# Kernel optimization log

Measured on AMD Instinct MI355X. Metric: run time of the kernel, lower is better.

Reference implementation:

```python
import jax, jax.numpy as jnp
import numpy as np

NUM_HEADS = 8
SIGMA = 1.0
LAMBDA_INIT = 0.1
GAMMA_INIT = 0.001


def _pos_encoding(H, W, d_model):
    # 2D sinusoidal encoding: first half encodes x (width), second half y (height)
    d = d_model // 2
    div = jnp.exp(jnp.arange(0, d, 2, dtype=jnp.float32) * (-np.log(10000.0) / d))
    xs = jnp.arange(W, dtype=jnp.float32)[:, None] * div  # (W, d//2)
    ys = jnp.arange(H, dtype=jnp.float32)[:, None] * div  # (H, d//2)
    pe_x = jnp.stack([jnp.sin(xs), jnp.cos(xs)], axis=-1).reshape(W, d)
    pe_y = jnp.stack([jnp.sin(ys), jnp.cos(ys)], axis=-1).reshape(H, d)
    pe = jnp.concatenate([
        jnp.broadcast_to(pe_x[None, :, :], (H, W, d)),
        jnp.broadcast_to(pe_y[:, None, :], (H, W, d)),
    ], axis=-1)
    return pe  # (H, W, d_model)


def _distance_map(H, W, sigma):
    # exp(-euclidean_dist / sigma) between all flattened pixel positions
    yy, xx = jnp.meshgrid(jnp.arange(H, dtype=jnp.float32), jnp.arange(W, dtype=jnp.float32), indexing='ij')
    coords = jnp.stack([yy.reshape(-1), xx.reshape(-1)], axis=-1)  # (HW, 2)
    d2 = jnp.sum((coords[:, None, :] - coords[None, :, :]) ** 2, axis=-1)
    return jnp.exp(-jnp.sqrt(d2) / sigma)  # (HW, HW)


def _conv1x1(x, w, b):
    # 1x1 conv == channel matmul; x: (B,C,H,W), w: (O,C), b: (O,)
    return jnp.einsum('bchw,oc->bohw', x, w) + b[None, :, None, None]


def setup_inputs() -> dict:
    key = jax.random.key(0)
    ks = jax.random.split(key, 9)
    B, C, H, W = 2, 256, 48, 48
    d_model = 256
    inp = {
        'x': jax.random.normal(ks[0], (B, C, H, W), dtype=jnp.float32),
        'Wq': jax.random.normal(ks[1], (d_model, C), dtype=jnp.float32) * 0.01,
        'bq': jnp.zeros((d_model,), dtype=jnp.float32),
        'Wk': jax.random.normal(ks[2], (d_model, C), dtype=jnp.float32) * 0.01,
        'bk': jnp.zeros((d_model,), dtype=jnp.float32),
        'Wv': jax.random.normal(ks[3], (d_model, C), dtype=jnp.float32) * 0.01,
        'bv': jnp.zeros((d_model,), dtype=jnp.float32),
        'Wo': jax.random.normal(ks[4], (C, d_model), dtype=jnp.float32) * 0.01,
        'bo': jnp.zeros((C,), dtype=jnp.float32),
        'lambda_dist': jnp.float32(LAMBDA_INIT),
        'gamma': jnp.float32(GAMMA_INIT),
    }
    return inp


def reference(x, Wq, bq, Wk, bk, Wv, bv, Wo, bo, lambda_dist, gamma):
    B, C, H, W = x.shape
    d_model = Wq.shape[0]
    d_k = d_model // NUM_HEADS
    pe = _pos_encoding(H, W, d_model).transpose(2, 0, 1)[None]  # (1, d_model, H, W)
    dm = _distance_map(H, W, SIGMA)                              # (HW, HW)

    q = _conv1x1(x, Wq, bq) + pe
    k = _conv1x1(x, Wk, bk) + pe
    v = _conv1x1(x, Wv, bv)

    def heads(t):
        return t.reshape(B, NUM_HEADS, d_k, H * W).transpose(0, 1, 3, 2)  # (B,h,HW,d_k)

    Q, K, V = heads(q), heads(k), heads(v)
    scores = jnp.einsum('bhnd,bhmd->bhnm', Q, K) / jnp.sqrt(jnp.float32(d_k))
    scores = scores + (lambda_dist * dm)[None, None]  # 'exp' distance prior bias
    attn = jax.nn.softmax(scores, axis=-1)
    out = jnp.einsum('bhnm,bhmd->bhnd', attn, V)
    out = out.transpose(0, 1, 3, 2).reshape(B, d_model, H, W)
    fused = gamma * out  # simple weighted fusion, single (self) branch
    return x + _conv1x1(fused, Wo, bo)
```

## Files before the change

kernel.cpp:

```cpp
#include <hip/hip_runtime.h>

#define HW 2304
#define SW 48
#define DMODEL 256
#define NHEADS 8
#define DK 32
#define BATCH 2

typedef unsigned short u16;
typedef __attribute__((ext_vector_type(8))) short short8;
typedef __attribute__((ext_vector_type(4))) float f32x4;

__device__ __forceinline__ float bf2f(u16 v) {
  union { unsigned int u; float f; } c; c.u = ((unsigned int)v) << 16; return c.f;
}
__device__ __forceinline__ float lo2f(unsigned int u) {
  union { unsigned int u; float f; } c; c.u = u << 16; return c.f;
}
__device__ __forceinline__ float hi2f(unsigned int u) {
  union { unsigned int u; float f; } c; c.u = u & 0xffff0000u; return c.f;
}
__device__ __forceinline__ u16 f2bf(float f) {
  union { unsigned int u; float f; } c; c.f = f;
  unsigned int u = c.u;
  unsigned int r = (u + 0x7FFFu + ((u >> 16) & 1u)) >> 16;
  return (u16)r;
}
__device__ __forceinline__ int div48(int n) { return (n * 87382) >> 22; }
__device__ __forceinline__ int swz(int row, int k) {
  return ((row >> 4) << 12) + ((k >> 3) << 7) + ((row & 15) << 3) + (k & 7);
}

__global__ __launch_bounds__(256) void eb_kernel(const float* __restrict__ lam_p,
                                                 u16* __restrict__ et) {
  int id = blockIdx.x * 256 + threadIdx.x;
  int flat = id * 8;
  int tile = flat >> 8;
  int within = flat & 255;
  int tm = tile / 144, tq = tile - tm * 144;
  int m = tm * 16 + (within >> 4);
  int q = tq * 16 + (within & 15);
  int ym = div48(m), xm = m - ym * SW;
  int yq = div48(q), xq = q - yq * SW;
  float lam = lam_p[0];
  float dy = (float)(yq - ym);
  float dy2 = dy * dy;
  u16 o[8];
#pragma unroll
  for (int j = 0; j < 8; ++j) {
    float dx = (float)(xq + j - xm);
    o[j] = f2bf(lam * __expf(-sqrtf(dy2 + dx * dx)));
  }
  *(uint4*)(et + flat) = *(const uint4*)o;
}

__global__ __launch_bounds__(256) void prep_kernel(
    const float* __restrict__ x,
    const float* __restrict__ Wq, const float* __restrict__ Wk,
    const float* __restrict__ Wv, const float* __restrict__ Wo,
    u16* __restrict__ xt, u16* __restrict__ Wb) {
  int bid = blockIdx.x;
  int t = threadIdx.x;
  if (bid < 288) {
    int b = bid / 144, r = bid % 144;
    int c0 = (r / 36) * 64, n0 = (r % 36) * 64;
    __shared__ u16 sh[64][72];
#pragma unroll
    for (int p = 0; p < 4; ++p) {
      int row = (t >> 4) + p * 16;
      int col4 = (t & 15) * 4;
      float4 v = *(const float4*)(x + (size_t)(b * DMODEL + c0 + row) * HW +
                                  n0 + col4);
      sh[col4 + 0][row] = f2bf(v.x);
      sh[col4 + 1][row] = f2bf(v.y);
      sh[col4 + 2][row] = f2bf(v.z);
      sh[col4 + 3][row] = f2bf(v.w);
    }
    __syncthreads();
    u16* xtb = xt + (size_t)b * HW * DMODEL;
#pragma unroll
    for (int q = 0; q < 2; ++q) {
      int nrow = t >> 2;
      int c8 = (t & 3) * 8 + q * 32;
      *(uint4*)(xtb + swz(n0 + nrow, c0 + c8)) = *(const uint4*)&sh[nrow][c8];
    }
  } else {
    int idx = (bid - 288) * 1024 + t * 4;
    int which = idx >> 16, off = idx & 65535;
    int m = off >> 8, k = off & 255;
    const float* src = (which == 0) ? Wq : (which == 1) ? Wk
                       : (which == 2) ? Wv : Wo;
    float4 v = *(const float4*)(src + off);
    ushort4 ov;
    ov.x = f2bf(v.x); ov.y = f2bf(v.y); ov.z = f2bf(v.z); ov.w = f2bf(v.w);
    *(ushort4*)(Wb + which * 65536 + swz(m, k)) = ov;
  }
}

__global__ __launch_bounds__(256) void qkv_kernel(
    const u16* __restrict__ Wb, const u16* __restrict__ xt,
    const float* __restrict__ bq, const float* __restrict__ bk,
    const float* __restrict__ bv,
    u16* __restrict__ qt, u16* __restrict__ ktb, u16* __restrict__ vb) {
  int t = threadIdx.x;
  int w = t >> 6, lane = t & 63, lo = lane & 15, quad = lane >> 4;
  int n0 = blockIdx.x * 64;
  int mb = blockIdx.y, b = blockIdx.z;
  int which = mb >> 2;
  int mrel0 = (mb & 3) * 64;
  const u16* A = Wb + which * 65536 + ((mrel0 + w * 16) >> 4) * 4096 + lo * 8;
  const float* bias = (which == 0) ? bq : (which == 1) ? bk : bv;
  const u16* Bx = xt + (size_t)b * HW * DMODEL + lo * 8;

  f32x4 acc[4] = {{0.f, 0.f, 0.f, 0.f}, {0.f, 0.f, 0.f, 0.f},
                  {0.f, 0.f, 0.f, 0.f}, {0.f, 0.f, 0.f, 0.f}};
#pragma unroll
  for (int k0 = 0; k0 < DMODEL; k0 += 32) {
    int kblk = ((k0 >> 3) + quad) << 7;
    short8 af = *(const short8*)(A + kblk);
#pragma unroll
    for (int nt = 0; nt < 4; ++nt) {
      short8 bf_ = *(const short8*)(Bx + ((n0 + nt * 16) >> 4) * 4096 + kblk);
      acc[nt] = __builtin_amdgcn_mfma_f32_16x16x32_bf16(af, bf_, acc[nt], 0, 0, 0);
    }
  }

  int mbase = mrel0 + w * 16 + quad * 4;
  if (which == 2) {
#pragma unroll
    for (int reg = 0; reg < 4; ++reg) {
      int mrel = mbase + reg;
      float bi = bias[mrel];
      u16* dst = vb + (size_t)(b * DMODEL + mrel) * HW + n0 + lo;
#pragma unroll
      for (int nt = 0; nt < 4; ++nt) dst[nt * 16] = f2bf(acc[nt][reg] + bi);
    }
  } else {
    float sc = (which == 0) ? 0.17677669529663687f : 1.0f;
    int h = mbase >> 5, d0 = mbase & 31;
    u16* base = ((which == 0) ? qt : ktb) + (size_t)(b * NHEADS + h) * HW * DK;
    float bi[4], dv[4];
    bool usecos[4], usey[4];
#pragma unroll
    for (int reg = 0; reg < 4; ++reg) {
      int mrel = mbase + reg;
      bi[reg] = bias[mrel];
      int oo = mrel & 127;
      dv[reg] = expf(-0.07195578415606394f * (float)(oo & ~1));
      usecos[reg] = (oo & 1);
      usey[reg] = (mrel >= 128);
    }
#pragma unroll
    for (int nt = 0; nt < 4; ++nt) {
      int n = n0 + nt * 16 + lo;
      int yy = div48(n), xx = n - yy * SW;
      ushort4 ov;
      float vals[4];
#pragma unroll
      for (int reg = 0; reg < 4; ++reg) {
        float tv = (usey[reg] ? (float)yy : (float)xx) * dv[reg];
        float pe = usecos[reg] ? cosf(tv) : sinf(tv);
        vals[reg] = (acc[nt][reg] + bi[reg] + pe) * sc;
      }
      ov.x = f2bf(vals[0]); ov.y = f2bf(vals[1]);
      ov.z = f2bf(vals[2]); ov.w = f2bf(vals[3]);
      *(ushort4*)(base + (size_t)n * DK + d0) = ov;
    }
  }
}

__global__ __launch_bounds__(256) void attn_kernel(
    const u16* __restrict__ qt, const u16* __restrict__ ktb,
    const u16* __restrict__ vb, const u16* __restrict__ et,
    u16* __restrict__ aot) {
  int t = threadIdx.x;
  int w = t >> 6;
  int lane = t & 63;
  int lo = lane & 15, quad = lane >> 4;
  int n0 = blockIdx.x * 64;
  int h = blockIdx.y, b = blockIdx.z;

  __shared__ u16 Ks[64 * 40];
  __shared__ u16 Vs[32 * 72];
  __shared__ u16 Ps[4 * 16 * 72];

  const u16* qtg = qt + (size_t)(b * NHEADS + h) * HW * DK;
  const u16* ktg = ktb + (size_t)(b * NHEADS + h) * HW * DK;
  const u16* vbg = vb + (size_t)(b * DMODEL + h * DK) * HW;

  short8 qf = *(const short8*)(qtg + (size_t)(n0 + w * 16 + lo) * DK + quad * 8);

  int tq = (n0 >> 4) + w;
  const u16* etw = et + (size_t)tq * 256 + lo * 16 + quad * 4;

  f32x4 o0 = {0.f, 0.f, 0.f, 0.f}, o1 = {0.f, 0.f, 0.f, 0.f};
  float lsum[4] = {0.f, 0.f, 0.f, 0.f};
  u16* psw = Ps + w * 16 * 72;

  for (int kt = 0; kt < 36; ++kt) {
    int m0 = kt * 64;
    __syncthreads();
    {
      int row = t >> 2, c8 = (t & 3) * 8;
      *(uint4*)&Ks[row * 40 + c8] =
          *(const uint4*)(ktg + (size_t)(m0 + row) * DK + c8);
      int dd = t >> 3, mo = (t & 7) * 8;
      *(uint4*)&Vs[dd * 72 + mo] =
          *(const uint4*)(vbg + (size_t)dd * HW + m0 + mo);
    }
    __syncthreads();

    uint2 ebv[4];
#pragma unroll
    for (int t4 = 0; t4 < 4; ++t4)
      ebv[t4] = *(const uint2*)(etw + (size_t)((m0 >> 4) + t4) * 36864);

    f32x4 s[4];
#pragma unroll
    for (int t4 = 0; t4 < 4; ++t4) {
      short8 kf = *(const short8*)&Ks[(t4 * 16 + lo) * 40 + quad * 8];
      f32x4 z = {0.f, 0.f, 0.f, 0.f};
      s[t4] = __builtin_amdgcn_mfma_f32_16x16x32_bf16(qf, kf, z, 0, 0, 0);
    }
#pragma unroll
    for (int t4 = 0; t4 < 4; ++t4) {
      float p0 = __expf(s[t4][0] + lo2f(ebv[t4].x));
      float p1 = __expf(s[t4][1] + hi2f(ebv[t4].x));
      float p2 = __expf(s[t4][2] + lo2f(ebv[t4].y));
      float p3 = __expf(s[t4][3] + hi2f(ebv[t4].y));
      lsum[0] += p0; lsum[1] += p1; lsum[2] += p2; lsum[3] += p3;
      psw[(quad * 4 + 0) * 72 + t4 * 16 + lo] = f2bf(p0);
      psw[(quad * 4 + 1) * 72 + t4 * 16 + lo] = f2bf(p1);
      psw[(quad * 4 + 2) * 72 + t4 * 16 + lo] = f2bf(p2);
      psw[(quad * 4 + 3) * 72 + t4 * 16 + lo] = f2bf(p3);
    }
#pragma unroll
    for (int ks = 0; ks < 2; ++ks) {
      short8 af = *(const short8*)&psw[lo * 72 + ks * 32 + quad * 8];
      short8 v0 = *(const short8*)&Vs[lo * 72 + ks * 32 + quad * 8];
      o0 = __builtin_amdgcn_mfma_f32_16x16x32_bf16(af, v0, o0, 0, 0, 0);
      short8 v1 = *(const short8*)&Vs[(16 + lo) * 72 + ks * 32 + quad * 8];
      o1 = __builtin_amdgcn_mfma_f32_16x16x32_bf16(af, v1, o1, 0, 0, 0);
    }
  }

#pragma unroll
  for (int d = 1; d < 16; d <<= 1) {
#pragma unroll
    for (int reg = 0; reg < 4; ++reg) lsum[reg] += __shfl_xor(lsum[reg], d);
  }

  u16* aog = aot + (size_t)b * HW * DMODEL;
#pragma unroll
  for (int reg = 0; reg < 4; ++reg) {
    int n = n0 + w * 16 + quad * 4 + reg;
    float inv = 1.0f / lsum[reg];
    aog[swz(n, h * DK + lo)] = f2bf(o0[reg] * inv);
    aog[swz(n, h * DK + 16 + lo)] = f2bf(o1[reg] * inv);
  }
}

__global__ __launch_bounds__(256) void out_kernel(
    const float* __restrict__ x, const u16* __restrict__ Wob,
    const float* __restrict__ bo, const float* __restrict__ gp,
    const u16* __restrict__ aot, float* __restrict__ out) {
  int t = threadIdx.x;
  int w = t >> 6, lane = t & 63, lo = lane & 15, quad = lane >> 4;
  int n0 = blockIdx.x * 64;
  int c0 = blockIdx.y * 64;
  int b = blockIdx.z;
  float gamma = gp[0];
  const u16* A = Wob + ((c0 + w * 16) >> 4) * 4096 + lo * 8;
  const u16* Ba = aot + (size_t)b * HW * DMODEL + lo * 8;

  f32x4 acc[4] = {{0.f, 0.f, 0.f, 0.f}, {0.f, 0.f, 0.f, 0.f},
                  {0.f, 0.f, 0.f, 0.f}, {0.f, 0.f, 0.f, 0.f}};
#pragma unroll
  for (int k0 = 0; k0 < DMODEL; k0 += 32) {
    int kblk = ((k0 >> 3) + quad) << 7;
    short8 af = *(const short8*)(A + kblk);
#pragma unroll
    for (int nt = 0; nt < 4; ++nt) {
      short8 bf_ = *(const short8*)(Ba + ((n0 + nt * 16) >> 4) * 4096 + kblk);
      acc[nt] = __builtin_amdgcn_mfma_f32_16x16x32_bf16(af, bf_, acc[nt], 0, 0, 0);
    }
  }

#pragma unroll
  for (int reg = 0; reg < 4; ++reg) {
    int c = c0 + w * 16 + quad * 4 + reg;
    float bi = bo[c];
    const float* xs = x + (size_t)(b * DMODEL + c) * HW + n0 + lo;
    float* os = out + (size_t)(b * DMODEL + c) * HW + n0 + lo;
#pragma unroll
    for (int nt = 0; nt < 4; ++nt)
      os[nt * 16] = xs[nt * 16] + gamma * acc[nt][reg] + bi;
  }
}

extern "C" void kernel_launch(void* const* d_in, const int* in_sizes, int n_in,
                              void* d_out, int out_size, void* d_ws,
                              size_t ws_size, hipStream_t stream) {
  const float* x   = (const float*)d_in[0];
  const float* Wq  = (const float*)d_in[1];
  const float* bq  = (const float*)d_in[2];
  const float* Wk  = (const float*)d_in[3];
  const float* bk  = (const float*)d_in[4];
  const float* Wv  = (const float*)d_in[5];
  const float* bv  = (const float*)d_in[6];
  const float* Wo  = (const float*)d_in[7];
  const float* bo  = (const float*)d_in[8];
  const float* lam = (const float*)d_in[9];
  const float* gam = (const float*)d_in[10];

  char* wsb = (char*)d_ws;
  u16* Wb  = (u16*)(wsb + 36864);
  u16* xt  = (u16*)(wsb + 561152);
  u16* aot = xt;
  u16* qt  = (u16*)(wsb + 2920448);
  u16* ktb = (u16*)(wsb + 5279744);
  u16* vb  = (u16*)(wsb + 7639040);
  u16* et  = (u16*)(wsb + 9998336);
  float* out = (float*)d_out;

  eb_kernel<<<dim3(2592), 256, 0, stream>>>(lam, et);
  prep_kernel<<<dim3(544), 256, 0, stream>>>(x, Wq, Wk, Wv, Wo, xt, Wb);
  qkv_kernel<<<dim3(36, 12, BATCH), 256, 0, stream>>>(Wb, xt, bq, bk, bv,
                                                      qt, ktb, vb);
  attn_kernel<<<dim3(36, NHEADS, BATCH), 256, 0, stream>>>(qt, ktb, vb, et,
                                                           aot);
  out_kernel<<<dim3(36, 4, BATCH), 256, 0, stream>>>(x, Wb + 3 * 65536, bo, gam,
                                                     aot, out);
}
```

Before: 151.3 us.

## Load K/V fragments straight into registers with double-buffered prefetch

The attention kernel no longer stages K and V tiles through shared memory with two block-wide barriers per tile. Each wave now loads its MFMA K and V fragments directly from global memory into registers. It alternates between two register buffers so the next tile's loads are in flight while the current tile is computed. The aim is to remove the barrier stalls and LDS round trips and to hide load latency. In exchange, each of the four waves re-reads the same K/V data, which relies on the caches, and register pressure rises. The final prefetch also reads one tile past the end of the sequence.

```diff
diff --git a/kernel.cpp b/kernel.cpp
--- a/kernel.cpp
+++ b/kernel.cpp
@@ -169,6 +169,22 @@
   }
 }
 
+__device__ __forceinline__ void ld_tile(const u16* __restrict__ ktg,
+                                        const u16* __restrict__ vbg, int m0,
+                                        int lo, int quad,
+                                        short8 kf[4], short8 vf[4]) {
+#pragma unroll
+  for (int t4 = 0; t4 < 4; ++t4)
+    kf[t4] = *(const short8*)(ktg + (size_t)(m0 + t4 * 16 + lo) * DK + quad * 8);
+#pragma unroll
+  for (int ks = 0; ks < 2; ++ks) {
+    vf[ks * 2 + 0] =
+        *(const short8*)(vbg + (size_t)lo * HW + m0 + ks * 32 + quad * 8);
+    vf[ks * 2 + 1] =
+        *(const short8*)(vbg + (size_t)(16 + lo) * HW + m0 + ks * 32 + quad * 8);
+  }
+}
+
 __global__ __launch_bounds__(256) void attn_kernel(
     const u16* __restrict__ qt, const u16* __restrict__ ktb,
     const u16* __restrict__ vb, const u16* __restrict__ et,
@@ -180,8 +196,6 @@
   int n0 = blockIdx.x * 64;
   int h = blockIdx.y, b = blockIdx.z;
 
-  __shared__ u16 Ks[64 * 40];
-  __shared__ u16 Vs[32 * 72];
   __shared__ u16 Ps[4 * 16 * 72];
 
   const u16* qtg = qt + (size_t)(b * NHEADS + h) * HW * DK;
@@ -197,52 +211,47 @@
   float lsum[4] = {0.f, 0.f, 0.f, 0.f};
   u16* psw = Ps + w * 16 * 72;
 
-  for (int kt = 0; kt < 36; ++kt) {
-    int m0 = kt * 64;
-    __syncthreads();
-    {
-      int row = t >> 2, c8 = (t & 3) * 8;
-      *(uint4*)&Ks[row * 40 + c8] =
-          *(const uint4*)(ktg + (size_t)(m0 + row) * DK + c8);
-      int dd = t >> 3, mo = (t & 7) * 8;
-      *(uint4*)&Vs[dd * 72 + mo] =
-          *(const uint4*)(vbg + (size_t)dd * HW + m0 + mo);
-    }
-    __syncthreads();
-
-    uint2 ebv[4];
-#pragma unroll
-    for (int t4 = 0; t4 < 4; ++t4)
-      ebv[t4] = *(const uint2*)(etw + (size_t)((m0 >> 4) + t4) * 36864);
-
-    f32x4 s[4];
-#pragma unroll
-    for (int t4 = 0; t4 < 4; ++t4) {
-      short8 kf = *(const short8*)&Ks[(t4 * 16 + lo) * 40 + quad * 8];
-      f32x4 z = {0.f, 0.f, 0.f, 0.f};
-      s[t4] = __builtin_amdgcn_mfma_f32_16x16x32_bf16(qf, kf, z, 0, 0, 0);
-    }
-#pragma unroll
-    for (int t4 = 0; t4 < 4; ++t4) {
-      float p0 = __expf(s[t4][0] + lo2f(ebv[t4].x));
-      float p1 = __expf(s[t4][1] + hi2f(ebv[t4].x));
-      float p2 = __expf(s[t4][2] + lo2f(ebv[t4].y));
-      float p3 = __expf(s[t4][3] + hi2f(ebv[t4].y));
-      lsum[0] += p0; lsum[1] += p1; lsum[2] += p2; lsum[3] += p3;
-      psw[(quad * 4 + 0) * 72 + t4 * 16 + lo] = f2bf(p0);
-      psw[(quad * 4 + 1) * 72 + t4 * 16 + lo] = f2bf(p1);
-      psw[(quad * 4 + 2) * 72 + t4 * 16 + lo] = f2bf(p2);
-      psw[(quad * 4 + 3) * 72 + t4 * 16 + lo] = f2bf(p3);
-    }
-#pragma unroll
-    for (int ks = 0; ks < 2; ++ks) {
-      short8 af = *(const short8*)&psw[lo * 72 + ks * 32 + quad * 8];
-      short8 v0 = *(const short8*)&Vs[lo * 72 + ks * 32 + quad * 8];
-      o0 = __builtin_amdgcn_mfma_f32_16x16x32_bf16(af, v0, o0, 0, 0, 0);
-      short8 v1 = *(const short8*)&Vs[(16 + lo) * 72 + ks * 32 + quad * 8];
-      o1 = __builtin_amdgcn_mfma_f32_16x16x32_bf16(af, v1, o1, 0, 0, 0);
-    }
-  }
+  short8 ka[4], va[4], kb[4], vbf[4];
+  ld_tile(ktg, vbg, 0, lo, quad, ka, va);
+
+#define ATTN_BODY(M0, KF, VF)                                                  \
+  {                                                                            \
+    const int m0_ = (M0);                                                      \
+    uint2 ebv[4];                                                              \
+    _Pragma("unroll") for (int t4 = 0; t4 < 4; ++t4) ebv[t4] =                 \
+        *(const uint2*)(etw + (size_t)((m0_ >> 4) + t4) * 36864);              \
+    f32x4 s[4];                                                                \
+    _Pragma("unroll") for (int t4 = 0; t4 < 4; ++t4) {                         \
+      f32x4 z = {0.f, 0.f, 0.f, 0.f};                                          \
+      s[t4] = __builtin_amdgcn_mfma_f32_16x16x32_bf16(qf, KF[t4], z, 0, 0, 0); \
+    }                                                                          \
+    _Pragma("unroll") for (int t4 = 0; t4 < 4; ++t4) {                         \
+      float p0 = __expf(s[t4][0] + lo2f(ebv[t4].x));                           \
+      float p1 = __expf(s[t4][1] + hi2f(ebv[t4].x));                           \
+      float p2 = __expf(s[t4][2] + lo2f(ebv[t4].y));                           \
+      float p3 = __expf(s[t4][3] + hi2f(ebv[t4].y));                           \
+      lsum[0] += p0; lsum[1] += p1; lsum[2] += p2; lsum[3] += p3;              \
+      psw[(quad * 4 + 0) * 72 + t4 * 16 + lo] = f2bf(p0);                      \
+      psw[(quad * 4 + 1) * 72 + t4 * 16 + lo] = f2bf(p1);                      \
+      psw[(quad * 4 + 2) * 72 + t4 * 16 + lo] = f2bf(p2);                      \
+      psw[(quad * 4 + 3) * 72 + t4 * 16 + lo] = f2bf(p3);                      \
+    }                                                                          \
+    _Pragma("unroll") for (int ks = 0; ks < 2; ++ks) {                         \
+      short8 af = *(const short8*)&psw[lo * 72 + ks * 32 + quad * 8];          \
+      o0 = __builtin_amdgcn_mfma_f32_16x16x32_bf16(af, VF[ks * 2 + 0], o0, 0,  \
+                                                   0, 0);                      \
+      o1 = __builtin_amdgcn_mfma_f32_16x16x32_bf16(af, VF[ks * 2 + 1], o1, 0,  \
+                                                   0, 0);                      \
+    }                                                                          \
+  }
+
+  for (int kt = 0; kt < 36; kt += 2) {
+    ld_tile(ktg, vbg, (kt + 1) * 64, lo, quad, kb, vbf);
+    ATTN_BODY(kt * 64, ka, va);
+    ld_tile(ktg, vbg, (kt + 2) * 64, lo, quad, ka, va);
+    ATTN_BODY((kt + 1) * 64, kb, vbf);
+  }
+#undef ATTN_BODY
 
 #pragma unroll
   for (int d = 1; d < 16; d <<= 1) {
```

Measured after the change: 189.0 us. +25.0%, slower.

## Split attention key range across two blocks and merge partials in reduce kernel

Applied to the files above, without the earlier changes.

The attention kernel now splits the 36 key tiles into two halves handled by separate blocks, doubling the grid to 1152 blocks. Each half writes unnormalised bf16 partial outputs and row sums to scratch space in the output buffer. A new reduce kernel adds the two partials and normalises them. The distance-bias kernel is also folded into the prep kernel, saving one launch. This targets low occupancy, since 576 blocks underfill the GPU, and pays for it with an extra launch, extra global traffic, and bf16 rounding of the partial results. The split has no max-rescaling, which matches the code before, so the softmax runs without max subtraction.

```diff
diff --git a/kernel.cpp b/kernel.cpp
--- a/kernel.cpp
+++ b/kernel.cpp
@@ -31,34 +31,12 @@
   return ((row >> 4) << 12) + ((k >> 3) << 7) + ((row & 15) << 3) + (k & 7);
 }
 
-__global__ __launch_bounds__(256) void eb_kernel(const float* __restrict__ lam_p,
-                                                 u16* __restrict__ et) {
-  int id = blockIdx.x * 256 + threadIdx.x;
-  int flat = id * 8;
-  int tile = flat >> 8;
-  int within = flat & 255;
-  int tm = tile / 144, tq = tile - tm * 144;
-  int m = tm * 16 + (within >> 4);
-  int q = tq * 16 + (within & 15);
-  int ym = div48(m), xm = m - ym * SW;
-  int yq = div48(q), xq = q - yq * SW;
-  float lam = lam_p[0];
-  float dy = (float)(yq - ym);
-  float dy2 = dy * dy;
-  u16 o[8];
-#pragma unroll
-  for (int j = 0; j < 8; ++j) {
-    float dx = (float)(xq + j - xm);
-    o[j] = f2bf(lam * __expf(-sqrtf(dy2 + dx * dx)));
-  }
-  *(uint4*)(et + flat) = *(const uint4*)o;
-}
-
 __global__ __launch_bounds__(256) void prep_kernel(
     const float* __restrict__ x,
     const float* __restrict__ Wq, const float* __restrict__ Wk,
     const float* __restrict__ Wv, const float* __restrict__ Wo,
-    u16* __restrict__ xt, u16* __restrict__ Wb) {
+    const float* __restrict__ lam_p,
+    u16* __restrict__ xt, u16* __restrict__ Wb, u16* __restrict__ et) {
   int bid = blockIdx.x;
   int t = threadIdx.x;
   if (bid < 288) {
@@ -84,7 +62,7 @@
       int c8 = (t & 3) * 8 + q * 32;
       *(uint4*)(xtb + swz(n0 + nrow, c0 + c8)) = *(const uint4*)&sh[nrow][c8];
     }
-  } else {
+  } else if (bid < 544) {
     int idx = (bid - 288) * 1024 + t * 4;
     int which = idx >> 16, off = idx & 65535;
     int m = off >> 8, k = off & 255;
@@ -94,6 +72,26 @@
     ushort4 ov;
     ov.x = f2bf(v.x); ov.y = f2bf(v.y); ov.z = f2bf(v.z); ov.w = f2bf(v.w);
     *(ushort4*)(Wb + which * 65536 + swz(m, k)) = ov;
+  } else {
+    int id = (bid - 544) * 256 + t;
+    int flat = id * 8;
+    int tile = flat >> 8;
+    int within = flat & 255;
+    int tm = tile / 144, tq = tile - tm * 144;
+    int m = tm * 16 + (within >> 4);
+    int q = tq * 16 + (within & 15);
+    int ym = div48(m), xm = m - ym * SW;
+    int yq = div48(q), xq = q - yq * SW;
+    float lam = lam_p[0];
+    float dy = (float)(yq - ym);
+    float dy2 = dy * dy;
+    u16 o[8];
+#pragma unroll
+    for (int j = 0; j < 8; ++j) {
+      float dx = (float)(xq + j - xm);
+      o[j] = f2bf(lam * __expf(-sqrtf(dy2 + dx * dx)));
+    }
+    *(uint4*)(et + flat) = *(const uint4*)o;
   }
 }
 
@@ -172,13 +170,14 @@
 __global__ __launch_bounds__(256) void attn_kernel(
     const u16* __restrict__ qt, const u16* __restrict__ ktb,
     const u16* __restrict__ vb, const u16* __restrict__ et,
-    u16* __restrict__ aot) {
+    u16* __restrict__ po_o, float* __restrict__ po_l) {
   int t = threadIdx.x;
   int w = t >> 6;
   int lane = t & 63;
   int lo = lane & 15, quad = lane >> 4;
   int n0 = blockIdx.x * 64;
-  int h = blockIdx.y, b = blockIdx.z;
+  int h = blockIdx.y >> 1, kh = blockIdx.y & 1;
+  int b = blockIdx.z;
 
   __shared__ u16 Ks[64 * 40];
   __shared__ u16 Vs[32 * 72];
@@ -197,7 +196,7 @@
   float lsum[4] = {0.f, 0.f, 0.f, 0.f};
   u16* psw = Ps + w * 16 * 72;
 
-  for (int kt = 0; kt < 36; ++kt) {
+  for (int kt = kh * 18; kt < kh * 18 + 18; ++kt) {
     int m0 = kt * 64;
     __syncthreads();
     {
@@ -250,13 +249,55 @@
     for (int reg = 0; reg < 4; ++reg) lsum[reg] += __shfl_xor(lsum[reg], d);
   }
 
+  int slot = (b * NHEADS + h) * 36 + blockIdx.x;
+  u16* pw = po_o + (size_t)(kh * 576 + slot) * 2048 + w * 512;
+  ushort4 s0, s1;
+  s0.x = f2bf(o0[0]); s0.y = f2bf(o0[1]); s0.z = f2bf(o0[2]); s0.w = f2bf(o0[3]);
+  s1.x = f2bf(o1[0]); s1.y = f2bf(o1[1]); s1.z = f2bf(o1[2]); s1.w = f2bf(o1[3]);
+  *(ushort4*)(pw + lane * 4) = s0;
+  *(ushort4*)(pw + 256 + lane * 4) = s1;
+  if (lo == 0) {
+    float4 lv = make_float4(lsum[0], lsum[1], lsum[2], lsum[3]);
+    *(float4*)(po_l + (size_t)(kh * 576 + slot) * 64 + w * 16 + quad * 4) = lv;
+  }
+}
+
+__global__ __launch_bounds__(256) void reduce_kernel(
+    const u16* __restrict__ po_o, const float* __restrict__ po_l,
+    u16* __restrict__ aot) {
+  int t = threadIdx.x;
+  int w = t >> 6, lane = t & 63, lo = lane & 15, quad = lane >> 4;
+  int qt_ = blockIdx.x, h = blockIdx.y, b = blockIdx.z;
+  int slot = (b * NHEADS + h) * 36 + qt_;
+
+  const u16* p0 = po_o + (size_t)slot * 2048 + w * 512;
+  const u16* p1 = p0 + 576 * 2048;
+  ushort4 a0 = *(const ushort4*)(p0 + lane * 4);
+  ushort4 b0 = *(const ushort4*)(p1 + lane * 4);
+  ushort4 a1 = *(const ushort4*)(p0 + 256 + lane * 4);
+  ushort4 b1 = *(const ushort4*)(p1 + 256 + lane * 4);
+
+  const float* l0p = po_l + (size_t)slot * 64 + w * 16 + quad * 4;
+  float4 l0 = *(const float4*)l0p;
+  float4 l1 = *(const float4*)(l0p + 576 * 64);
+  float inv[4];
+  inv[0] = 1.0f / (l0.x + l1.x);
+  inv[1] = 1.0f / (l0.y + l1.y);
+  inv[2] = 1.0f / (l0.z + l1.z);
+  inv[3] = 1.0f / (l0.w + l1.w);
+
+  u16 av0[4] = {(u16)a0.x, (u16)a0.y, (u16)a0.z, (u16)a0.w};
+  u16 bv0[4] = {(u16)b0.x, (u16)b0.y, (u16)b0.z, (u16)b0.w};
+  u16 av1[4] = {(u16)a1.x, (u16)a1.y, (u16)a1.z, (u16)a1.w};
+  u16 bv1[4] = {(u16)b1.x, (u16)b1.y, (u16)b1.z, (u16)b1.w};
+
   u16* aog = aot + (size_t)b * HW * DMODEL;
 #pragma unroll
   for (int reg = 0; reg < 4; ++reg) {
-    int n = n0 + w * 16 + quad * 4 + reg;
-    float inv = 1.0f / lsum[reg];
-    aog[swz(n, h * DK + lo)] = f2bf(o0[reg] * inv);
-    aog[swz(n, h * DK + 16 + lo)] = f2bf(o1[reg] * inv);
+    int n = qt_ * 64 + w * 16 + quad * 4 + reg;
+    aog[swz(n, h * DK + lo)] = f2bf((bf2f(av0[reg]) + bf2f(bv0[reg])) * inv[reg]);
+    aog[swz(n, h * DK + 16 + lo)] =
+        f2bf((bf2f(av1[reg]) + bf2f(bv1[reg])) * inv[reg]);
   }
 }
 
@@ -321,14 +362,17 @@
   u16* ktb = (u16*)(wsb + 5279744);
   u16* vb  = (u16*)(wsb + 7639040);
   u16* et  = (u16*)(wsb + 9998336);
+  float* po_l = (float*)(wsb + 20615168);
+  u16* po_o = (u16*)d_out;
   float* out = (float*)d_out;
 
-  eb_kernel<<<dim3(2592), 256, 0, stream>>>(lam, et);
-  prep_kernel<<<dim3(544), 256, 0, stream>>>(x, Wq, Wk, Wv, Wo, xt, Wb);
+  prep_kernel<<<dim3(3136), 256, 0, stream>>>(x, Wq, Wk, Wv, Wo, lam,
+                                              xt, Wb, et);
   qkv_kernel<<<dim3(36, 12, BATCH), 256, 0, stream>>>(Wb, xt, bq, bk, bv,
                                                       qt, ktb, vb);
-  attn_kernel<<<dim3(36, NHEADS, BATCH), 256, 0, stream>>>(qt, ktb, vb, et,
-                                                           aot);
+  attn_kernel<<<dim3(36, 16, BATCH), 256, 0, stream>>>(qt, ktb, vb, et,
+                                                       po_o, po_l);
+  reduce_kernel<<<dim3(36, 8, BATCH), 256, 0, stream>>>(po_o, po_l, aot);
   out_kernel<<<dim3(36, 4, BATCH), 256, 0, stream>>>(x, Wb + 3 * 65536, bo, gam,
                                                      aot, out);
 }
```

Result: faster. 137.8 us (-8.9%).
